# Kernel tuning notes

Hardware: AMD Instinct MI355X
Metric: run time of the kernel (lower is better)

Reference implementation:

```python
import jax, jax.numpy as jnp
import numpy as np

B, L, D = 4, 2048, 1024
H, DK, DV = 8, 128, 128
LN_EPS = 1e-5


def setup_inputs() -> dict:
    key = jax.random.key(0)
    ks = jax.random.split(key, 8)
    def xavier(k, shape):
        std = float(np.sqrt(2.0 / (shape[0] + shape[1])))
        return jax.random.normal(k, shape, dtype=jnp.float32) * std
    return {
        "q": jax.random.normal(ks[0], (B, L, D), dtype=jnp.float32),
        "k": jax.random.normal(ks[1], (B, L, D), dtype=jnp.float32),
        "v": jax.random.normal(ks[2], (B, L, D), dtype=jnp.float32),
        "mask": jnp.ones((B, L), dtype=jnp.int32),
        "Wq": xavier(ks[3], (H * DK, D)),
        "Wk": xavier(ks[4], (H * DK, D)),
        "Wv": xavier(ks[5], (H * DV, D)),
        "Wo": xavier(ks[6], (D, H * DV)),
        "gamma": jnp.ones((D,), dtype=jnp.float32),
        "beta": jnp.zeros((D,), dtype=jnp.float32),
    }


def reference(q, k, v, mask, Wq, Wk, Wv, Wo, gamma, beta):
    # dropout layers are identity in eval mode
    residual = q
    # project and split heads -> [H, B, L, dk] (matches permute(2,0,1,3))
    qh = (q @ Wq.T).reshape(B, L, H, DK).transpose(2, 0, 1, 3)
    kh = (k @ Wk.T).reshape(B, L, H, DK).transpose(2, 0, 1, 3)
    vh = (v @ Wv.T).reshape(B, L, H, DV).transpose(2, 0, 1, 3)
    scale = jnp.sqrt(jnp.asarray(DK, dtype=qh.dtype))
    scores = jnp.einsum('hbqd,hbkd->hbqk', qh, kh) / scale  # [H,B,Lq,Lk]
    neg_inf = jnp.asarray(-jnp.inf, dtype=scores.dtype)
    scores = jnp.where(mask[None, :, None, :] == 0, neg_inf, scores)
    attn = jax.nn.softmax(scores, axis=-1)
    out = jnp.einsum('hbqk,hbkd->hbqd', attn, vh)  # [H,B,Lq,dv]
    out = out.transpose(1, 2, 0, 3).reshape(B, L, H * DV)
    out = out @ Wo.T
    x = out + residual
    mu = jnp.mean(x, axis=-1, keepdims=True)
    var = jnp.var(x, axis=-1, keepdims=True)
    y = (x - mu) * jax.lax.rsqrt(var + LN_EPS) * gamma + beta
    return y, attn.reshape(H * B, L, L)
```

## Files before the change

### kernel.cpp

```cpp
#include <hip/hip_runtime.h>
#include <hip/hip_bf16.h>


typedef __hip_bfloat16 bf16;
typedef __attribute__((ext_vector_type(8))) short bf16x8;
typedef __attribute__((ext_vector_type(4))) float f32x4;

#define MFMA16(a, b, c) __builtin_amdgcn_mfma_f32_16x16x32_bf16((a), (b), (c), 0, 0, 0)


static constexpr int LSEQ = 2048;
static constexpr float SCALE = 0.08838834764831845f;
static constexpr size_t Y_ELEMS = 8388608;
static constexpr size_t ATTN_PER_HB = 4194304;

__global__ void detect_dtype(const unsigned* __restrict__ g, int* __restrict__ flag) {
  if (threadIdx.x == 0 && blockIdx.x == 0) *flag = (g[0] == 0x3F800000u) ? 1 : 0;
}

__global__ __launch_bounds__(256) void cast_bf16(const void* __restrict__ src,
                                                 bf16* __restrict__ dst,
                                                 const int* __restrict__ flagp) {
  const int i = (blockIdx.x * 256 + threadIdx.x) * 4;
  if (*flagp) {
    const float4 v = *(const float4*)((const float*)src + i);
    alignas(8) bf16 t[4] = {__float2bfloat16(v.x), __float2bfloat16(v.y),
                            __float2bfloat16(v.z), __float2bfloat16(v.w)};
    *(uint2*)(dst + i) = *(const uint2*)t;
  } else {
    *(uint2*)(dst + i) = *(const uint2*)((const bf16*)src + i);
  }
}

__global__ __launch_bounds__(256) void cast_f32(const void* __restrict__ src,
                                                float* __restrict__ dst,
                                                const int* __restrict__ flagp) {
  const int i = blockIdx.x * 256 + threadIdx.x;
  dst[i] = (*flagp) ? ((const float*)src)[i] : __bfloat162float(((const bf16*)src)[i]);
}

template <int MODE>
__global__ __launch_bounds__(256) void gemm_xwT(const bf16* __restrict__ X,
                                                const bf16* __restrict__ W,
                                                void* __restrict__ outp,
                                                const bf16* __restrict__ resid) {
  const int lane = threadIdx.x & 63;
  const int wv   = threadIdx.x >> 6;
  const int c16  = lane & 15;
  const int quad = lane >> 4;
  const int m0 = blockIdx.x * 64 + wv * 16;
  const int n0 = blockIdx.y * 64;
  const int K = 1024;

  f32x4 acc0 = {0.f, 0.f, 0.f, 0.f}, acc1 = acc0, acc2 = acc0, acc3 = acc0;
  const bf16* xrow = X + (size_t)(m0 + c16) * K + quad * 8;
  const bf16* wrow = W + (size_t)(n0 + c16) * K + quad * 8;

  for (int k0 = 0; k0 < K; k0 += 32) {
    bf16x8 a  = *(const bf16x8*)(xrow + k0);
    bf16x8 b0 = *(const bf16x8*)(wrow + k0);
    bf16x8 b1 = *(const bf16x8*)(wrow + 16 * K + k0);
    bf16x8 b2 = *(const bf16x8*)(wrow + 32 * K + k0);
    bf16x8 b3 = *(const bf16x8*)(wrow + 48 * K + k0);
    acc0 = MFMA16(a, b0, acc0);
    acc1 = MFMA16(a, b1, acc1);
    acc2 = MFMA16(a, b2, acc2);
    acc3 = MFMA16(a, b3, acc3);
  }

  f32x4 accs[4] = {acc0, acc1, acc2, acc3};
#pragma unroll
  for (int t = 0; t < 4; ++t) {
#pragma unroll
    for (int r = 0; r < 4; ++r) {
      const int m = m0 + quad * 4 + r;
      const int n = n0 + t * 16 + c16;
      const float v = accs[t][r];
      if (MODE == 0) {
        const int h = n >> 7, d = n & 127, bb = m >> 11, l = m & 2047;
        ((bf16*)outp)[((size_t)((h * 4 + bb) * 2048 + l)) * 128 + d] = __float2bfloat16(v);
      } else if (MODE == 2) {
        const int h = n >> 7, d = n & 127, bb = m >> 11, l = m & 2047;
        ((bf16*)outp)[((size_t)((h * 4 + bb) * 128 + d)) * 2048 + l] = __float2bfloat16(v);
      } else {
        const float rr = __bfloat162float(resid[(size_t)m * 1024 + n]);
        ((float*)outp)[(size_t)m * 1024 + n] = v + rr;
      }
    }
  }
}

__global__ __launch_bounds__(256) void attn_softmax(const bf16* __restrict__ qh,
                                                    const bf16* __restrict__ kh,
                                                    const int* __restrict__ mask,
                                                    void* __restrict__ dout,
                                                    const int* __restrict__ flagp) {
  __shared__ float wm[4][16], wl[4][16], fm[16], fl[16];

  const int f32 = *flagp;
  const int hb = blockIdx.y;
  const int bb = hb & 3;
  const int q0 = blockIdx.x * 16;
  const int lane = threadIdx.x & 63;
  const int wv   = threadIdx.x >> 6;
  const int c16  = lane & 15;
  const int quad = lane >> 4;

  const bf16* Q  = qh + (size_t)hb * LSEQ * 128;
  const bf16* Kh = kh + (size_t)hb * LSEQ * 128;

  bf16x8 afrag[4];
#pragma unroll
  for (int kk = 0; kk < 4; ++kk)
    afrag[kk] = *(const bf16x8*)(Q + (size_t)(q0 + c16) * 128 + kk * 32 + quad * 8);

  f32x4 sv[32];
#pragma unroll
  for (int t = 0; t < 32; ++t) {
    const int col0 = wv * 512 + t * 16;
    f32x4 s = {0.f, 0.f, 0.f, 0.f};
#pragma unroll
    for (int kk = 0; kk < 4; ++kk) {
      bf16x8 bfr = *(const bf16x8*)(Kh + (size_t)(col0 + c16) * 128 + kk * 32 + quad * 8);
      s = MFMA16(afrag[kk], bfr, s);
    }
    const int mk = mask[bb * 2048 + col0 + c16];
#pragma unroll
    for (int r = 0; r < 4; ++r) {
      float x = s[r] * SCALE;
      s[r] = (mk == 0) ? -1e30f : x;
    }
    sv[t] = s;
  }

  float mloc[4], lloc[4];
#pragma unroll
  for (int r = 0; r < 4; ++r) {
    float m = -1e30f;
#pragma unroll
    for (int t = 0; t < 32; ++t) m = fmaxf(m, sv[t][r]);
#pragma unroll
    for (int off = 1; off < 16; off <<= 1) m = fmaxf(m, __shfl_xor(m, off));
    float l = 0.f;
#pragma unroll
    for (int t = 0; t < 32; ++t) l += __expf(sv[t][r] - m);
#pragma unroll
    for (int off = 1; off < 16; off <<= 1) l += __shfl_xor(l, off);
    mloc[r] = m;
    lloc[r] = l;
  }
  if (c16 == 0) {
#pragma unroll
    for (int r = 0; r < 4; ++r) {
      wm[wv][quad * 4 + r] = mloc[r];
      wl[wv][quad * 4 + r] = lloc[r];
    }
  }
  __syncthreads();
  if (threadIdx.x < 16) {
    float M = wm[0][threadIdx.x];
    for (int w = 1; w < 4; ++w) M = fmaxf(M, wm[w][threadIdx.x]);
    float Ls = 0.f;
    for (int w = 0; w < 4; ++w) Ls += wl[w][threadIdx.x] * __expf(wm[w][threadIdx.x] - M);
    fm[threadIdx.x] = M;
    fl[threadIdx.x] = 1.0f / Ls;
  }
  __syncthreads();

  float myM[4], myL[4];
#pragma unroll
  for (int r = 0; r < 4; ++r) {
    myM[r] = fm[quad * 4 + r];
    myL[r] = fl[quad * 4 + r];
  }

  float* aF = (float*)dout + Y_ELEMS + (size_t)hb * ATTN_PER_HB;
  bf16*  aH = (bf16*)dout + Y_ELEMS + (size_t)hb * ATTN_PER_HB;
#pragma unroll
  for (int t = 0; t < 32; ++t) {
    const int col0 = wv * 512 + t * 16;
#pragma unroll
    for (int r = 0; r < 4; ++r) {
      const float p = __expf(sv[t][r] - myM[r]) * myL[r];
      const size_t idx = (size_t)(q0 + quad * 4 + r) * 2048 + col0 + c16;
      if (f32) aF[idx] = p;
      else     aH[idx] = __float2bfloat16(p);
    }
  }
}

__global__ __launch_bounds__(256) void attn_v(const void* __restrict__ dout,
                                              const bf16* __restrict__ vt,
                                              bf16* __restrict__ O,
                                              const int* __restrict__ flagp) {
  const int f32 = *flagp;
  const int hb = blockIdx.y;
  const int lane = threadIdx.x & 63;
  const int wv   = threadIdx.x >> 6;
  const int c16  = lane & 15;
  const int quad = lane >> 4;
  const int m0 = blockIdx.x * 64 + wv * 16;

  const bf16* Vt = vt + (size_t)hb * 128 * LSEQ;
  const bf16* vrow = Vt + (size_t)c16 * LSEQ + quad * 8;

  f32x4 acc[8];
#pragma unroll
  for (int t = 0; t < 8; ++t) acc[t] = f32x4{0.f, 0.f, 0.f, 0.f};

  if (f32) {
    const float* A = (const float*)dout + Y_ELEMS + (size_t)hb * ATTN_PER_HB;
    const float* arow = A + (size_t)(m0 + c16) * 2048 + quad * 8;
    for (int k0 = 0; k0 < 2048; k0 += 32) {
      const float4 p0 = *(const float4*)(arow + k0);
      const float4 p1 = *(const float4*)(arow + k0 + 4);
      alignas(16) bf16 t8[8] = {
          __float2bfloat16(p0.x), __float2bfloat16(p0.y), __float2bfloat16(p0.z),
          __float2bfloat16(p0.w), __float2bfloat16(p1.x), __float2bfloat16(p1.y),
          __float2bfloat16(p1.z), __float2bfloat16(p1.w)};
      const bf16x8 a = *(const bf16x8*)t8;
#pragma unroll
      for (int t = 0; t < 8; ++t) {
        const bf16x8 b = *(const bf16x8*)(vrow + (size_t)t * 16 * LSEQ + k0);
        acc[t] = MFMA16(a, b, acc[t]);
      }
    }
  } else {
    const bf16* A = (const bf16*)dout + Y_ELEMS + (size_t)hb * ATTN_PER_HB;
    const bf16* arow = A + (size_t)(m0 + c16) * 2048 + quad * 8;
    for (int k0 = 0; k0 < 2048; k0 += 32) {
      const bf16x8 a = *(const bf16x8*)(arow + k0);
#pragma unroll
      for (int t = 0; t < 8; ++t) {
        const bf16x8 b = *(const bf16x8*)(vrow + (size_t)t * 16 * LSEQ + k0);
        acc[t] = MFMA16(a, b, acc[t]);
      }
    }
  }

  const int bb = hb & 3, h = hb >> 2;
#pragma unroll
  for (int t = 0; t < 8; ++t) {
#pragma unroll
    for (int r = 0; r < 4; ++r) {
      const int m = m0 + quad * 4 + r;
      const int n = t * 16 + c16;
      O[(size_t)(bb * 2048 + m) * 1024 + h * 128 + n] = __float2bfloat16(acc[t][r]);
    }
  }
}

__global__ __launch_bounds__(256) void layernorm(const float* __restrict__ x,
                                                 const float* __restrict__ gamma,
                                                 const float* __restrict__ beta,
                                                 void* __restrict__ y,
                                                 const int* __restrict__ flagp) {
  __shared__ float ss[4], ss2[4];
  const int row = blockIdx.x;
  const float4 v = ((const float4*)(x + (size_t)row * 1024))[threadIdx.x];
  float s  = v.x + v.y + v.z + v.w;
  float s2 = v.x * v.x + v.y * v.y + v.z * v.z + v.w * v.w;
#pragma unroll
  for (int off = 32; off >= 1; off >>= 1) {
    s  += __shfl_xor(s, off);
    s2 += __shfl_xor(s2, off);
  }
  if ((threadIdx.x & 63) == 0) {
    ss[threadIdx.x >> 6]  = s;
    ss2[threadIdx.x >> 6] = s2;
  }
  __syncthreads();
  const float tot  = ss[0] + ss[1] + ss[2] + ss[3];
  const float tot2 = ss2[0] + ss2[1] + ss2[2] + ss2[3];
  const float mu = tot * (1.0f / 1024.0f);
  const float var = tot2 * (1.0f / 1024.0f) - mu * mu;
  const float rs = rsqrtf(var + 1e-5f);

  const int c = threadIdx.x * 4;
  const float vv[4] = {v.x, v.y, v.z, v.w};
  float o[4];
#pragma unroll
  for (int i = 0; i < 4; ++i)
    o[i] = (vv[i] - mu) * rs * gamma[c + i] + beta[c + i];

  if (*flagp) {
    *(float4*)((float*)y + (size_t)row * 1024 + c) = make_float4(o[0], o[1], o[2], o[3]);
  } else {
    alignas(8) bf16 ob[4] = {__float2bfloat16(o[0]), __float2bfloat16(o[1]),
                             __float2bfloat16(o[2]), __float2bfloat16(o[3])};
    *(uint2*)((bf16*)y + (size_t)row * 1024 + c) = *(const uint2*)ob;
  }
}

extern "C" void kernel_launch(void* const* d_in, const int* in_sizes, int n_in,
                              void* d_out, int out_size, void* d_ws, size_t ws_size,
                              hipStream_t stream) {
  const void* q     = d_in[0];
  const void* k     = d_in[1];
  const void* v     = d_in[2];
  const int*  mask  = (const int*)d_in[3];
  const void* Wq    = d_in[4];
  const void* Wk    = d_in[5];
  const void* Wv    = d_in[6];
  const void* Wo    = d_in[7];
  const void* gamma = d_in[8];
  const void* beta  = d_in[9];

  char* ws = (char*)d_ws;
  bf16* qb  = (bf16*)(ws);
  bf16* kb  = (bf16*)(ws + 16777216);
  bf16* vb  = (bf16*)(ws + 33554432);
  bf16* wqb = (bf16*)(ws + 50331648);
  bf16* wkb = (bf16*)(ws + 52428800);
  bf16* wvb = (bf16*)(ws + 54525952);
  bf16* wob = (bf16*)(ws + 56623104);
  bf16* qh  = (bf16*)(ws + 58720256);
  bf16* kh  = (bf16*)(ws + 75497472);
  bf16* vt  = (bf16*)(ws + 92274688);
  bf16* o   = (bf16*)(ws + 109051904);
  float* gf = (float*)(ws + 125829120);
  float* bfb = (float*)(ws + 125833216);
  int* flag = (int*)(ws + 125837312);
  float* x  = (float*)(ws + 16777216);

  detect_dtype<<<1, 64, 0, stream>>>((const unsigned*)gamma, flag);

  cast_bf16<<<8192, 256, 0, stream>>>(q, qb, flag);
  cast_bf16<<<8192, 256, 0, stream>>>(k, kb, flag);
  cast_bf16<<<8192, 256, 0, stream>>>(v, vb, flag);
  cast_bf16<<<1024, 256, 0, stream>>>(Wq, wqb, flag);
  cast_bf16<<<1024, 256, 0, stream>>>(Wk, wkb, flag);
  cast_bf16<<<1024, 256, 0, stream>>>(Wv, wvb, flag);
  cast_bf16<<<1024, 256, 0, stream>>>(Wo, wob, flag);
  cast_f32<<<4, 256, 0, stream>>>(gamma, gf, flag);
  cast_f32<<<4, 256, 0, stream>>>(beta, bfb, flag);

  const dim3 gridP(8192 / 64, 1024 / 64);
  gemm_xwT<0><<<gridP, 256, 0, stream>>>(qb, wqb, (void*)qh, nullptr);
  gemm_xwT<0><<<gridP, 256, 0, stream>>>(kb, wkb, (void*)kh, nullptr);
  gemm_xwT<2><<<gridP, 256, 0, stream>>>(vb, wvb, (void*)vt, nullptr);

  attn_softmax<<<dim3(2048 / 16, 32), 256, 0, stream>>>(qh, kh, mask, d_out, flag);

  attn_v<<<dim3(2048 / 64, 32), 256, 0, stream>>>(d_out, vt, o, flag);

  gemm_xwT<3><<<gridP, 256, 0, stream>>>(o, wob, (void*)x, qb);

  layernorm<<<8192, 256, 0, stream>>>(x, gf, bfb, d_out, flag);
}
```

Baseline: 1.753 ms.

## Fuse softmax and attention-times-V into one kernel using register probabilities

```diff
diff --git a/kernel.cpp b/kernel.cpp
--- a/kernel.cpp
+++ b/kernel.cpp
@@ -4,7 +4,9 @@
 
 typedef __hip_bfloat16 bf16;
 typedef __attribute__((ext_vector_type(8))) short bf16x8;
+typedef __attribute__((ext_vector_type(4))) short bf16x4;
 typedef __attribute__((ext_vector_type(4))) float f32x4;
+typedef __attribute__((ext_vector_type(2))) unsigned int u32x2;
 
 #define MFMA16(a, b, c) __builtin_amdgcn_mfma_f32_16x16x32_bf16((a), (b), (c), 0, 0, 0)
 
@@ -13,6 +15,11 @@
 static constexpr float SCALE = 0.08838834764831845f;
 static constexpr size_t Y_ELEMS = 8388608;
 static constexpr size_t ATTN_PER_HB = 4194304;
+
+static __device__ inline short bf16bits(float x) {
+  __hip_bfloat16 h = __float2bfloat16(x);
+  return *reinterpret_cast<short*>(&h);
+}
 
 __global__ void detect_dtype(const unsigned* __restrict__ g, int* __restrict__ flag) {
   if (threadIdx.x == 0 && blockIdx.x == 0) *flag = (g[0] == 0x3F800000u) ? 1 : 0;
@@ -90,16 +97,20 @@
   }
 }
 
-__global__ __launch_bounds__(256) void attn_softmax(const bf16* __restrict__ qh,
-                                                    const bf16* __restrict__ kh,
-                                                    const int* __restrict__ mask,
-                                                    void* __restrict__ dout,
-                                                    const int* __restrict__ flagp) {
+__global__ __launch_bounds__(256, 2) void attn_fused(const bf16* __restrict__ qh,
+                                                     const bf16* __restrict__ kh,
+                                                     const bf16* __restrict__ vt,
+                                                     const int* __restrict__ mask,
+                                                     void* __restrict__ dout,
+                                                     bf16* __restrict__ O,
+                                                     const int* __restrict__ flagp) {
   __shared__ float wm[4][16], wl[4][16], fm[16], fl[16];
+  __shared__ float OL[4][16][132];
 
   const int f32 = *flagp;
   const int hb = blockIdx.y;
   const int bb = hb & 3;
+  const int h  = hb >> 2;
   const int q0 = blockIdx.x * 16;
   const int lane = threadIdx.x & 63;
   const int wv   = threadIdx.x >> 6;
@@ -108,11 +119,12 @@
 
   const bf16* Q  = qh + (size_t)hb * LSEQ * 128;
   const bf16* Kh = kh + (size_t)hb * LSEQ * 128;
-
-  bf16x8 afrag[4];
+  const bf16* Vt = vt + (size_t)hb * 128 * LSEQ;
+
+  bf16x8 qfrag[4];
 #pragma unroll
   for (int kk = 0; kk < 4; ++kk)
-    afrag[kk] = *(const bf16x8*)(Q + (size_t)(q0 + c16) * 128 + kk * 32 + quad * 8);
+    qfrag[kk] = *(const bf16x8*)(Q + (size_t)(q0 + c16) * 128 + kk * 32 + quad * 8);
 
   f32x4 sv[32];
 #pragma unroll
@@ -121,40 +133,37 @@
     f32x4 s = {0.f, 0.f, 0.f, 0.f};
 #pragma unroll
     for (int kk = 0; kk < 4; ++kk) {
-      bf16x8 bfr = *(const bf16x8*)(Kh + (size_t)(col0 + c16) * 128 + kk * 32 + quad * 8);
-      s = MFMA16(afrag[kk], bfr, s);
-    }
-    const int mk = mask[bb * 2048 + col0 + c16];
+      bf16x8 kfr = *(const bf16x8*)(Kh + (size_t)(col0 + c16) * 128 + kk * 32 + quad * 8);
+      s = MFMA16(kfr, qfrag[kk], s);
+    }
+    const int4 mk4 = *(const int4*)(mask + bb * 2048 + col0 + quad * 4);
+    const int mks[4] = {mk4.x, mk4.y, mk4.z, mk4.w};
 #pragma unroll
     for (int r = 0; r < 4; ++r) {
       float x = s[r] * SCALE;
-      s[r] = (mk == 0) ? -1e30f : x;
+      s[r] = (mks[r] == 0) ? -1e30f : x;
     }
     sv[t] = s;
   }
 
-  float mloc[4], lloc[4];
-#pragma unroll
-  for (int r = 0; r < 4; ++r) {
-    float m = -1e30f;
-#pragma unroll
-    for (int t = 0; t < 32; ++t) m = fmaxf(m, sv[t][r]);
-#pragma unroll
-    for (int off = 1; off < 16; off <<= 1) m = fmaxf(m, __shfl_xor(m, off));
-    float l = 0.f;
-#pragma unroll
-    for (int t = 0; t < 32; ++t) l += __expf(sv[t][r] - m);
-#pragma unroll
-    for (int off = 1; off < 16; off <<= 1) l += __shfl_xor(l, off);
-    mloc[r] = m;
-    lloc[r] = l;
-  }
-  if (c16 == 0) {
-#pragma unroll
-    for (int r = 0; r < 4; ++r) {
-      wm[wv][quad * 4 + r] = mloc[r];
-      wl[wv][quad * 4 + r] = lloc[r];
-    }
+  float m = -1e30f;
+#pragma unroll
+  for (int t = 0; t < 32; ++t)
+#pragma unroll
+    for (int r = 0; r < 4; ++r) m = fmaxf(m, sv[t][r]);
+  m = fmaxf(m, __shfl_xor(m, 16));
+  m = fmaxf(m, __shfl_xor(m, 32));
+  float l = 0.f;
+#pragma unroll
+  for (int t = 0; t < 32; ++t)
+#pragma unroll
+    for (int r = 0; r < 4; ++r) l += __expf(sv[t][r] - m);
+  l += __shfl_xor(l, 16);
+  l += __shfl_xor(l, 32);
+
+  if (quad == 0) {
+    wm[wv][c16] = m;
+    wl[wv][c16] = l;
   }
   __syncthreads();
   if (threadIdx.x < 16) {
@@ -166,88 +175,69 @@
     fl[threadIdx.x] = 1.0f / Ls;
   }
   __syncthreads();
-
-  float myM[4], myL[4];
-#pragma unroll
-  for (int r = 0; r < 4; ++r) {
-    myM[r] = fm[quad * 4 + r];
-    myL[r] = fl[quad * 4 + r];
-  }
+  const float myM = fm[c16];
+  const float myL = fl[c16];
 
   float* aF = (float*)dout + Y_ELEMS + (size_t)hb * ATTN_PER_HB;
   bf16*  aH = (bf16*)dout + Y_ELEMS + (size_t)hb * ATTN_PER_HB;
-#pragma unroll
-  for (int t = 0; t < 32; ++t) {
-    const int col0 = wv * 512 + t * 16;
-#pragma unroll
-    for (int r = 0; r < 4; ++r) {
-      const float p = __expf(sv[t][r] - myM[r]) * myL[r];
-      const size_t idx = (size_t)(q0 + quad * 4 + r) * 2048 + col0 + c16;
-      if (f32) aF[idx] = p;
-      else     aH[idx] = __float2bfloat16(p);
-    }
-  }
-}
-
-__global__ __launch_bounds__(256) void attn_v(const void* __restrict__ dout,
-                                              const bf16* __restrict__ vt,
-                                              bf16* __restrict__ O,
-                                              const int* __restrict__ flagp) {
-  const int f32 = *flagp;
-  const int hb = blockIdx.y;
-  const int lane = threadIdx.x & 63;
-  const int wv   = threadIdx.x >> 6;
-  const int c16  = lane & 15;
-  const int quad = lane >> 4;
-  const int m0 = blockIdx.x * 64 + wv * 16;
-
-  const bf16* Vt = vt + (size_t)hb * 128 * LSEQ;
-  const bf16* vrow = Vt + (size_t)c16 * LSEQ + quad * 8;
 
   f32x4 acc[8];
 #pragma unroll
-  for (int t = 0; t < 8; ++t) acc[t] = f32x4{0.f, 0.f, 0.f, 0.f};
-
-  if (f32) {
-    const float* A = (const float*)dout + Y_ELEMS + (size_t)hb * ATTN_PER_HB;
-    const float* arow = A + (size_t)(m0 + c16) * 2048 + quad * 8;
-    for (int k0 = 0; k0 < 2048; k0 += 32) {
-      const float4 p0 = *(const float4*)(arow + k0);
-      const float4 p1 = *(const float4*)(arow + k0 + 4);
-      alignas(16) bf16 t8[8] = {
-          __float2bfloat16(p0.x), __float2bfloat16(p0.y), __float2bfloat16(p0.z),
-          __float2bfloat16(p0.w), __float2bfloat16(p1.x), __float2bfloat16(p1.y),
-          __float2bfloat16(p1.z), __float2bfloat16(p1.w)};
-      const bf16x8 a = *(const bf16x8*)t8;
-#pragma unroll
-      for (int t = 0; t < 8; ++t) {
-        const bf16x8 b = *(const bf16x8*)(vrow + (size_t)t * 16 * LSEQ + k0);
-        acc[t] = MFMA16(a, b, acc[t]);
+  for (int dt = 0; dt < 8; ++dt) acc[dt] = f32x4{0.f, 0.f, 0.f, 0.f};
+
+#pragma unroll
+  for (int c = 0; c < 16; ++c) {
+    bf16x8 pfrag;
+#pragma unroll
+    for (int half = 0; half < 2; ++half) {
+      const int tt = c * 2 + half;
+      f32x4 pv;
+#pragma unroll
+      for (int r = 0; r < 4; ++r) {
+        const float p = __expf(sv[tt][r] - myM) * myL;
+        pv[r] = p;
+        pfrag[half * 4 + r] = bf16bits(p);
       }
-    }
-  } else {
-    const bf16* A = (const bf16*)dout + Y_ELEMS + (size_t)hb * ATTN_PER_HB;
-    const bf16* arow = A + (size_t)(m0 + c16) * 2048 + quad * 8;
-    for (int k0 = 0; k0 < 2048; k0 += 32) {
-      const bf16x8 a = *(const bf16x8*)(arow + k0);
-#pragma unroll
-      for (int t = 0; t < 8; ++t) {
-        const bf16x8 b = *(const bf16x8*)(vrow + (size_t)t * 16 * LSEQ + k0);
-        acc[t] = MFMA16(a, b, acc[t]);
+      const size_t aidx = (size_t)(q0 + c16) * 2048 + (size_t)(wv * 512 + tt * 16 + quad * 4);
+      if (f32) {
+        __builtin_nontemporal_store(pv, (f32x4*)(aF + aidx));
+      } else {
+        u32x2 w2;
+        w2[0] = (unsigned)(unsigned short)pfrag[half * 4 + 0] |
+                ((unsigned)(unsigned short)pfrag[half * 4 + 1] << 16);
+        w2[1] = (unsigned)(unsigned short)pfrag[half * 4 + 2] |
+                ((unsigned)(unsigned short)pfrag[half * 4 + 3] << 16);
+        __builtin_nontemporal_store(w2, (u32x2*)(aH + aidx));
       }
     }
-  }
-
-  const int bb = hb & 3, h = hb >> 2;
-#pragma unroll
-  for (int t = 0; t < 8; ++t) {
-#pragma unroll
-    for (int r = 0; r < 4; ++r) {
-      const int m = m0 + quad * 4 + r;
-      const int n = t * 16 + c16;
-      O[(size_t)(bb * 2048 + m) * 1024 + h * 128 + n] = __float2bfloat16(acc[t][r]);
-    }
-  }
+    const int kbase = wv * 512 + c * 32;
+#pragma unroll
+    for (int dt = 0; dt < 8; ++dt) {
+      const bf16* vp = Vt + (size_t)(dt * 16 + c16) * 2048 + kbase + quad * 4;
+      const bf16x4 lo = *(const bf16x4*)vp;
+      const bf16x4 hi = *(const bf16x4*)(vp + 16);
+      bf16x8 vf;
+      vf[0] = lo[0]; vf[1] = lo[1]; vf[2] = lo[2]; vf[3] = lo[3];
+      vf[4] = hi[0]; vf[5] = hi[1]; vf[6] = hi[2]; vf[7] = hi[3];
+      acc[dt] = MFMA16(vf, pfrag, acc[dt]);
+    }
+  }
+
+#pragma unroll
+  for (int dt = 0; dt < 8; ++dt)
+    *(f32x4*)&OL[wv][c16][dt * 16 + quad * 4] = acc[dt];
+  __syncthreads();
+
+  const int qq = threadIdx.x >> 4;
+  const int d0 = (threadIdx.x & 15) * 8;
+  alignas(16) bf16 ob[8];
+#pragma unroll
+  for (int i = 0; i < 8; ++i) {
+    const float s4 = OL[0][qq][d0 + i] + OL[1][qq][d0 + i] +
+                     OL[2][qq][d0 + i] + OL[3][qq][d0 + i];
+    ob[i] = __float2bfloat16(s4);
+  }
+  *(uint4*)(O + (size_t)(bb * 2048 + q0 + qq) * 1024 + h * 128 + d0) = *(const uint4*)ob;
 }
 
 __global__ __launch_bounds__(256) void layernorm(const float* __restrict__ x,
@@ -340,9 +330,7 @@
   gemm_xwT<0><<<gridP, 256, 0, stream>>>(kb, wkb, (void*)kh, nullptr);
   gemm_xwT<2><<<gridP, 256, 0, stream>>>(vb, wvb, (void*)vt, nullptr);
 
-  attn_softmax<<<dim3(2048 / 16, 32), 256, 0, stream>>>(qh, kh, mask, d_out, flag);
-
-  attn_v<<<dim3(2048 / 64, 32), 256, 0, stream>>>(d_out, vt, o, flag);
+  attn_fused<<<dim3(2048 / 16, 32), 256, 0, stream>>>(qh, kh, vt, mask, d_out, o, flag);
 
   gemm_xwT<3><<<gridP, 256, 0, stream>>>(o, wob, (void*)x, qb);
 
```

Result: slower. 1.853 ms (+5.7%).
